# Kernel optimization log

Measured on AMD Instinct MI355X. Metric: run time of the kernel, lower is better.

Reference implementation:

```python
import jax, jax.numpy as jnp
import numpy as np

DIM = 1024
HID = 2048
OUT = 1024
NE = 8
TOPK = 2

def _xavier(key, shape):
    fan_in, fan_out = shape[-2], shape[-1]
    lim = jnp.sqrt(6.0 / (fan_in + fan_out))
    return jax.random.uniform(key, shape, jnp.float32, -lim, lim)

def setup_inputs() -> dict:
    key = jax.random.key(0)
    ks = jax.random.split(key, 8)
    X = jax.random.normal(ks[0], (4, 1024, DIM), jnp.float32)
    # stacked expert params: [NE, ...]
    W1 = _xavier(ks[1], (NE, DIM, HID))
    W3 = _xavier(ks[2], (NE, DIM, HID))
    W2 = _xavier(ks[3], (NE, HID, OUT))
    b1 = jnp.zeros((NE, HID), jnp.float32)
    b3 = jnp.zeros((NE, HID), jnp.float32)
    b2 = jnp.zeros((NE, OUT), jnp.float32)
    Wg = _xavier(ks[4], (DIM, NE))
    bg = jnp.zeros((NE,), jnp.float32)
    Wf = _xavier(ks[5], (OUT, OUT))
    bf = jnp.zeros((OUT,), jnp.float32)
    return {"X": X, "W1": W1, "b1": b1, "W3": W3, "b3": b3, "W2": W2, "b2": b2,
            "Wg": Wg, "bg": bg, "Wf": Wf, "bf": bf}

def reference(X, W1, b1, W3, b3, W2, b2, Wg, bg, Wf, bf):
    # gating: [B,S,E]
    gating = jax.nn.softmax(X @ Wg + bg, axis=-1)
    # top-k via argsort (matches original: ascending sort, take last k)
    top_k_indices = jnp.argsort(gating, axis=-1)[..., -TOPK:]  # [B,S,K]
    # dense all-expert SwiGLU FFN: [B,S,E,O]
    h1 = jnp.einsum('bsd,edh->bseh', X, W1) + b1  # [B,S,E,H]
    h3 = jnp.einsum('bsd,edh->bseh', X, W3) + b3
    h = jax.nn.silu(h1 * h3)
    expert_outputs = jnp.einsum('bseh,eho->bseo', h, W2) + b2  # [B,S,E,O]
    # gather top-k expert outputs
    topk_out = jnp.take_along_axis(expert_outputs, top_k_indices[..., None], axis=2)  # [B,S,K,O]
    topk_w = jnp.take_along_axis(gating, top_k_indices, axis=-1)  # [B,S,K]
    mixed = jnp.sum(topk_w[..., None] * topk_out, axis=2)  # [B,S,O]
    return mixed @ Wf + bf
```

## Files before the change

### kernel.cpp

```cpp
#include <hip/hip_runtime.h>

#define DIM  1024
#define HID  2048
#define OUTD 1024
#define NE   8
#define NTOK 4096

using bf16x8 = __attribute__((ext_vector_type(8))) short;
using f32x4  = __attribute__((ext_vector_type(4))) float;

__device__ __forceinline__ unsigned short f2bf(float f) {
  unsigned int u = __builtin_bit_cast(unsigned int, f);
  u += 0x7fff + ((u >> 16) & 1);
  return (unsigned short)(u >> 16);
}

__device__ __forceinline__ void gload16(const void* g, void* l) {
  __builtin_amdgcn_global_load_lds(
      (const __attribute__((address_space(1))) void*)g,
      (__attribute__((address_space(3))) void*)l, 16, 0, 0);
}

__global__ void tcast_kernel(const float* __restrict__ in,
                             unsigned short* __restrict__ out, int R, int C) {
  __shared__ float tile[32][33];
  size_t zo = (size_t)blockIdx.z * R * C;
  int c0 = blockIdx.x * 32, r0 = blockIdx.y * 32;
  int tx = threadIdx.x & 31, ty = threadIdx.x >> 5;
#pragma unroll
  for (int j = 0; j < 4; j++) {
    int r = ty + j * 8;
    tile[r][tx] = in[zo + (size_t)(r0 + r) * C + c0 + tx];
  }
  __syncthreads();
  int c = threadIdx.x >> 3, q = threadIdx.x & 7;
  ushort4 u;
  u.x = f2bf(tile[q * 4 + 0][c]); u.y = f2bf(tile[q * 4 + 1][c]);
  u.z = f2bf(tile[q * 4 + 2][c]); u.w = f2bf(tile[q * 4 + 3][c]);
  *(ushort4*)&out[zo + (size_t)(c0 + c) * R + r0 + q * 4] = u;
}

__global__ void tcast_i_kernel(const float* __restrict__ W1,
                               const float* __restrict__ W3,
                               unsigned short* __restrict__ out) {
  __shared__ float tile[32][33];
  int z = blockIdx.z, e = z & 7, s = z >> 3;
  const float* inp = (s ? W3 : W1) + (size_t)e * DIM * HID;
  unsigned short* op = out + (size_t)e * 2 * HID * DIM;
  int c0 = blockIdx.x * 32, r0 = blockIdx.y * 32;
  int tx = threadIdx.x & 31, ty = threadIdx.x >> 5;
#pragma unroll
  for (int j = 0; j < 4; j++) {
    int r = ty + j * 8;
    tile[r][tx] = inp[(size_t)(r0 + r) * HID + c0 + tx];
  }
  __syncthreads();
  int c = threadIdx.x >> 3, q = threadIdx.x & 7;
  int h = c0 + c;
  int orow = 32 * (h >> 4) + 16 * s + (h & 15);
  ushort4 u;
  u.x = f2bf(tile[q * 4 + 0][c]); u.y = f2bf(tile[q * 4 + 1][c]);
  u.z = f2bf(tile[q * 4 + 2][c]); u.w = f2bf(tile[q * 4 + 3][c]);
  *(ushort4*)&op[(size_t)orow * DIM + r0 + q * 4] = u;
}

__global__ __launch_bounds__(256) void gating_kernel(
    const float* __restrict__ X, const float* __restrict__ Wg,
    const float* __restrict__ bg, unsigned short* __restrict__ Xb,
    int* __restrict__ topk_pack, float* __restrict__ topk_w,
    int* __restrict__ blkcnt) {
  __shared__ float wgs[NE][DIM];
  __shared__ int hist[NE];
  const int tid = threadIdx.x;
  for (int d = tid; d < DIM; d += 256) {
#pragma unroll
    for (int e = 0; e < NE; e++) wgs[e][d] = Wg[d * NE + e];
  }
  if (tid < NE) hist[tid] = 0;
  __syncthreads();
  const int wave = tid >> 6, lane = tid & 63;
  for (int tk = wave; tk < 32; tk += 4) {
    const int t = blockIdx.x * 32 + tk;
    const float* xr = X + (size_t)t * DIM;
    {
      const float4* xp = (const float4*)(xr + lane * 16);
      float4 v0 = xp[0], v1 = xp[1], v2 = xp[2], v3 = xp[3];
      uint4 w0, w1;
      w0.x = f2bf(v0.x) | ((unsigned)f2bf(v0.y) << 16);
      w0.y = f2bf(v0.z) | ((unsigned)f2bf(v0.w) << 16);
      w0.z = f2bf(v1.x) | ((unsigned)f2bf(v1.y) << 16);
      w0.w = f2bf(v1.z) | ((unsigned)f2bf(v1.w) << 16);
      w1.x = f2bf(v2.x) | ((unsigned)f2bf(v2.y) << 16);
      w1.y = f2bf(v2.z) | ((unsigned)f2bf(v2.w) << 16);
      w1.z = f2bf(v3.x) | ((unsigned)f2bf(v3.y) << 16);
      w1.w = f2bf(v3.z) | ((unsigned)f2bf(v3.w) << 16);
      uint4* op = (uint4*)(Xb + (size_t)t * DIM + lane * 16);
      op[0] = w0; op[1] = w1;
    }
    float acc[NE];
#pragma unroll
    for (int e = 0; e < NE; e++) acc[e] = 0.f;
#pragma unroll
    for (int j = 0; j < 16; j++) {
      float xv = xr[lane + j * 64];
#pragma unroll
      for (int e = 0; e < NE; e++) acc[e] += xv * wgs[e][lane + j * 64];
    }
#pragma unroll
    for (int e = 0; e < NE; e++) {
#pragma unroll
      for (int off = 32; off > 0; off >>= 1) acc[e] += __shfl_xor(acc[e], off, 64);
    }
    if (lane == 0) {
      float p[NE];
      float mx = -1e30f;
#pragma unroll
      for (int e = 0; e < NE; e++) { p[e] = acc[e] + bg[e]; mx = fmaxf(mx, p[e]); }
      float s = 0.f;
#pragma unroll
      for (int e = 0; e < NE; e++) { p[e] = expf(p[e] - mx); s += p[e]; }
      float inv = 1.f / s;
#pragma unroll
      for (int e = 0; e < NE; e++) p[e] *= inv;
      int i1 = 0; float v1 = p[0];
#pragma unroll
      for (int e = 1; e < NE; e++) if (p[e] >= v1) { v1 = p[e]; i1 = e; }
      int i2 = (i1 == 0) ? 1 : 0; float v2 = p[i2];
#pragma unroll
      for (int e = 0; e < NE; e++) {
        if (e == i1) continue;
        if (p[e] >= v2 && e != i2) { v2 = p[e]; i2 = e; }
      }
      topk_pack[t] = i1 | (i2 << 4);
      topk_w[t * 2 + 0] = v1; topk_w[t * 2 + 1] = v2;
      atomicAdd(&hist[i1], 1); atomicAdd(&hist[i2], 1);
    }
  }
  __syncthreads();
  if (tid < NE) blkcnt[blockIdx.x * NE + tid] = hist[tid];
}

__global__ void prefix_kernel(const int* __restrict__ blkcnt, int* __restrict__ counts,
                              int* __restrict__ row_start, int* __restrict__ tp,
                              int* __restrict__ base) {
  const int lane = threadIdx.x;
  int tot[NE];
#pragma unroll
  for (int e = 0; e < NE; e++) {
    int s = blkcnt[lane * NE + e] + blkcnt[(lane + 64) * NE + e];
#pragma unroll
    for (int off = 32; off > 0; off >>= 1) s += __shfl_xor(s, off, 64);
    tot[e] = s;
  }
  int rsv[NE]; int s = 0, t = 0;
#pragma unroll
  for (int e = 0; e < NE; e++) {
    rsv[e] = s;
    if (lane == e) { counts[e] = tot[e]; row_start[e] = s; }
    if (lane == e) tp[e] = t;
    s += tot[e]; t += (tot[e] + 127) >> 7;
  }
  if (lane == 0) tp[NE] = t;
#pragma unroll
  for (int e = 0; e < NE; e++) {
    int c0 = blkcnt[(2 * lane) * NE + e], c1 = blkcnt[(2 * lane + 1) * NE + e];
    int s2 = c0 + c1, scan = s2;
#pragma unroll
    for (int off = 1; off < 64; off <<= 1) {
      int v = __shfl_up(scan, off, 64);
      if (lane >= off) scan += v;
    }
    int excl = scan - s2 + rsv[e];
    base[(2 * lane) * NE + e] = excl;
    base[(2 * lane + 1) * NE + e] = excl + c0;
  }
}

__global__ void scatter_kernel(const int* __restrict__ topk_pack, const int* __restrict__ base,
                               int* __restrict__ list) {
  __shared__ int lofs[NE];
  const int blk = blockIdx.x, tid = threadIdx.x;
  if (tid < NE) lofs[tid] = base[blk * NE + tid];
  __syncthreads();
  if (tid < 32) {
    int t = blk * 32 + tid;
    int pk = topk_pack[t];
    int e1 = pk & 15, e2 = (pk >> 4) & 15;
    int p1 = atomicAdd(&lofs[e1], 1);
    list[p1] = t << 1;
    int p2 = atomicAdd(&lofs[e2], 1);
    list[p2] = (t << 1) | 1;
  }
}

__global__ __launch_bounds__(256, 3) void ffn_a_kernel(
    const unsigned short* __restrict__ Xb,
    const unsigned short* __restrict__ W13t,
    const float* __restrict__ b1, const float* __restrict__ b3,
    const int* __restrict__ counts, const int* __restrict__ row_start,
    const int* __restrict__ tp, const int* __restrict__ list,
    unsigned short* __restrict__ h_buf) {
  __shared__ unsigned short As[128 * 64];
  __shared__ unsigned short Bs[128 * 64];
  const int bid = blockIdx.x;
  const int xcd = bid & 7, r = bid >> 3;
  const int grp = r >> 5, rr2 = r & 31;
  const int by = grp * 8 + (rr2 & 7);
  const int bx = xcd * 4 + (rr2 >> 3);
  if (by >= tp[NE]) return;
  int e = 0;
#pragma unroll
  for (int k = 1; k < NE; k++) if (by >= tp[k]) e = k;
  const int ne = counts[e], rs = row_start[e];
  const int m0 = (by - tp[e]) * 128;
  const int n0 = bx * 128;

  const int tid = threadIdx.x;
  const int wave = tid >> 6, lane = tid & 63;
  const int lr = lane & 15, lk = lane >> 4;
  const int wm = (wave >> 1) * 64, wn = (wave & 1) * 64;

  const int scs = ((lane & 7) ^ (lane >> 3)) * 8;
  const unsigned short* asrc[4];
  const unsigned short* bsrc[4];
#pragma unroll
  for (int i = 0; i < 4; i++) {
    int sr = (wave * 4 + i) * 8 + (lane >> 3);
    int rr = m0 + sr; if (rr >= ne) rr = m0;
    int tok = list[rs + rr] >> 1;
    asrc[i] = Xb + (size_t)tok * DIM + scs;
    bsrc[i] = W13t + ((size_t)e * 2 * HID + n0 + sr) * DIM + scs;
  }

  f32x4 acc[4][4];
  const f32x4 zero = {0.f, 0.f, 0.f, 0.f};
#pragma unroll
  for (int m = 0; m < 4; m++)
#pragma unroll
    for (int n = 0; n < 4; n++) acc[m][n] = zero;

  const int sx = lr & 7;

  for (int k0 = 0; k0 < DIM; k0 += 64) {
#pragma unroll
    for (int i = 0; i < 4; i++) {
      gload16(asrc[i] + k0, &As[(wave * 4 + i) * 512]);
      gload16(bsrc[i] + k0, &Bs[(wave * 4 + i) * 512]);
    }
    __syncthreads();
#pragma unroll
    for (int kk = 0; kk < 2; kk++) {
      const int sl = ((kk * 4 + lk) ^ sx) * 8;
      bf16x8 a[4], b[4];
#pragma unroll
      for (int m = 0; m < 4; m++)
        a[m] = *(const bf16x8*)&As[(wm + m * 16 + lr) * 64 + sl];
#pragma unroll
      for (int n = 0; n < 4; n++)
        b[n] = *(const bf16x8*)&Bs[(wn + n * 16 + lr) * 64 + sl];
#pragma unroll
      for (int m = 0; m < 4; m++)
#pragma unroll
        for (int n = 0; n < 4; n++)
          acc[m][n] = __builtin_amdgcn_mfma_f32_16x16x32_bf16(a[m], b[n], acc[m][n], 0, 0, 0);
    }
    __syncthreads();
  }

  const int hq = (n0 + wn) >> 5;
#pragma unroll
  for (int g = 0; g < 2; g++) {
    int h = (hq + g) * 16 + lr;
    float b1v = b1[e * HID + h];
    float b3v = b3[e * HID + h];
#pragma unroll
    for (int m = 0; m < 4; m++) {
#pragma unroll
      for (int j = 0; j < 4; j++) {
        int rr = m0 + wm + m * 16 + lk * 4 + j;
        if (rr < ne) {
          float h1 = acc[m][2 * g][j] + b1v;
          float h3 = acc[m][2 * g + 1][j] + b3v;
          float v = h1 * h3;
          h_buf[(size_t)(rs + rr) * HID + h] = f2bf(v / (1.f + expf(-v)));
        }
      }
    }
  }
}

__global__ __launch_bounds__(256, 3) void ffn_b_kernel(
    const unsigned short* __restrict__ h_buf,
    const unsigned short* __restrict__ W2t,
    const float* __restrict__ b2,
    const int* __restrict__ counts, const int* __restrict__ row_start,
    const int* __restrict__ tp, const int* __restrict__ list,
    const float* __restrict__ topk_w, float* __restrict__ o_buf) {
  __shared__ unsigned short As[128 * 64];
  __shared__ unsigned short Bs[128 * 64];
  const int bid = blockIdx.x;
  const int xcd = bid & 7, r = bid >> 3;
  const int grp = r / 24, rr2 = r % 24;
  const int by = xcd * 9 + grp * 3 + (rr2 % 3);
  const int bx = rr2 / 3;
  if (by >= tp[NE]) return;
  int e = 0;
#pragma unroll
  for (int k = 1; k < NE; k++) if (by >= tp[k]) e = k;
  const int ne = counts[e], rs = row_start[e];
  const int m0 = (by - tp[e]) * 128;
  const int n0 = bx * 128;

  const int tid = threadIdx.x;
  const int wave = tid >> 6, lane = tid & 63;
  const int lr = lane & 15, lk = lane >> 4;
  const int wm = (wave >> 1) * 64, wn = (wave & 1) * 64;

  const int scs = ((lane & 7) ^ (lane >> 3)) * 8;
  const unsigned short* asrc[4];
  const unsigned short* bsrc[4];
#pragma unroll
  for (int i = 0; i < 4; i++) {
    int sr = (wave * 4 + i) * 8 + (lane >> 3);
    asrc[i] = h_buf + (size_t)(rs + m0 + sr) * HID + scs;
    bsrc[i] = W2t + ((size_t)e * OUTD + n0 + sr) * HID + scs;
  }

  f32x4 acc[4][4];
  const f32x4 zero = {0.f, 0.f, 0.f, 0.f};
#pragma unroll
  for (int m = 0; m < 4; m++)
#pragma unroll
    for (int n = 0; n < 4; n++) acc[m][n] = zero;

  const int sx = lr & 7;

  for (int k0 = 0; k0 < HID; k0 += 64) {
#pragma unroll
    for (int i = 0; i < 4; i++) {
      gload16(asrc[i] + k0, &As[(wave * 4 + i) * 512]);
      gload16(bsrc[i] + k0, &Bs[(wave * 4 + i) * 512]);
    }
    __syncthreads();
#pragma unroll
    for (int kk = 0; kk < 2; kk++) {
      const int sl = ((kk * 4 + lk) ^ sx) * 8;
      bf16x8 a[4], b[4];
#pragma unroll
      for (int m = 0; m < 4; m++)
        a[m] = *(const bf16x8*)&As[(wm + m * 16 + lr) * 64 + sl];
#pragma unroll
      for (int n = 0; n < 4; n++)
        b[n] = *(const bf16x8*)&Bs[(wn + n * 16 + lr) * 64 + sl];
#pragma unroll
      for (int m = 0; m < 4; m++)
#pragma unroll
        for (int n = 0; n < 4; n++)
          acc[m][n] = __builtin_amdgcn_mfma_f32_16x16x32_bf16(a[m], b[n], acc[m][n], 0, 0, 0);
    }
    __syncthreads();
  }

#pragma unroll
  for (int n = 0; n < 4; n++) {
    int col = n0 + wn + n * 16 + lr;
    float b2v = b2[e * OUTD + col];
#pragma unroll
    for (int m = 0; m < 4; m++) {
#pragma unroll
      for (int j = 0; j < 4; j++) {
        int rr = m0 + wm + m * 16 + lk * 4 + j;
        if (rr < ne) {
          int entry = list[rs + rr];
          float w = topk_w[entry];
          o_buf[(size_t)entry * OUTD + col] = w * (acc[m][n][j] + b2v);
        }
      }
    }
  }
}

__global__ __launch_bounds__(256) void final_kernel(
    const float* __restrict__ o_buf, const unsigned short* __restrict__ Wft,
    const float* __restrict__ bfv, float* __restrict__ out) {
  const int m0 = blockIdx.y * 128, n0 = blockIdx.x * 128;

  __shared__ unsigned short As[128 * 64];
  __shared__ unsigned short Bs[128 * 64];

  const int tid = threadIdx.x;
  const int wave = tid >> 6, lane = tid & 63;
  const int lrow = lane >> 3;
  const int lcol = (lane & 7) * 8;

  const unsigned short* bsrc[4];
#pragma unroll
  for (int i = 0; i < 4; i++) {
    int sr = (wave * 4 + i) * 8 + lrow;
    bsrc[i] = Wft + (size_t)(n0 + sr) * DIM + lcol;
  }

  const int wm = (wave >> 1) * 64, wn = (wave & 1) * 64;
  const int lr = lane & 15, lk = lane >> 4;

  f32x4 acc[4][4];
  const f32x4 zero = {0.f, 0.f, 0.f, 0.f};
#pragma unroll
  for (int m = 0; m < 4; m++)
#pragma unroll
    for (int n = 0; n < 4; n++) acc[m][n] = zero;

  for (int k0 = 0; k0 < DIM; k0 += 64) {
#pragma unroll
    for (int g = 0; g < 8; g++) {
      int idx = g * 256 + tid;
      int r = idx >> 4;
      int c4 = (idx & 15) * 4;
      const float4 v0 = *(const float4*)&o_buf[(size_t)(m0 + r) * 2 * OUTD + k0 + c4];
      const float4 v1 = *(const float4*)&o_buf[(size_t)(m0 + r) * 2 * OUTD + OUTD + k0 + c4];
      ushort4 u;
      u.x = f2bf(v0.x + v1.x); u.y = f2bf(v0.y + v1.y);
      u.z = f2bf(v0.z + v1.z); u.w = f2bf(v0.w + v1.w);
      *(ushort4*)&As[r * 64 + c4] = u;
    }
#pragma unroll
    for (int i = 0; i < 4; i++) gload16(bsrc[i] + k0, &Bs[(wave * 4 + i) * 512]);
    __syncthreads();
#pragma unroll
    for (int kk = 0; kk < 2; kk++) {
      bf16x8 a[4], b[4];
#pragma unroll
      for (int m = 0; m < 4; m++)
        a[m] = *(const bf16x8*)&As[(wm + m * 16 + lr) * 64 + kk * 32 + lk * 8];
#pragma unroll
      for (int n = 0; n < 4; n++)
        b[n] = *(const bf16x8*)&Bs[(wn + n * 16 + lr) * 64 + kk * 32 + lk * 8];
#pragma unroll
      for (int m = 0; m < 4; m++)
#pragma unroll
        for (int n = 0; n < 4; n++)
          acc[m][n] = __builtin_amdgcn_mfma_f32_16x16x32_bf16(a[m], b[n], acc[m][n], 0, 0, 0);
    }
    __syncthreads();
  }

#pragma unroll
  for (int n = 0; n < 4; n++) {
    int col = n0 + wn + n * 16 + lr;
    float bv = bfv[col];
#pragma unroll
    for (int m = 0; m < 4; m++) {
#pragma unroll
      for (int j = 0; j < 4; j++) {
        int r = m0 + wm + m * 16 + lk * 4 + j;
        out[(size_t)r * OUTD + col] = acc[m][n][j] + bv;
      }
    }
  }
}

extern "C" void kernel_launch(void* const* d_in, const int* in_sizes, int n_in,
                              void* d_out, int out_size, void* d_ws, size_t ws_size,
                              hipStream_t stream) {
  const float* X   = (const float*)d_in[0];
  const float* W1  = (const float*)d_in[1];
  const float* b1  = (const float*)d_in[2];
  const float* W3  = (const float*)d_in[3];
  const float* b3  = (const float*)d_in[4];
  const float* W2  = (const float*)d_in[5];
  const float* b2  = (const float*)d_in[6];
  const float* Wg  = (const float*)d_in[7];
  const float* bg  = (const float*)d_in[8];
  const float* Wf  = (const float*)d_in[9];
  const float* bfv = (const float*)d_in[10];
  float* out = (float*)d_out;

  char* p = (char*)d_ws;
  auto alloc = [&](size_t bytes) { char* r = p; p += (bytes + 255) & ~(size_t)255; return r; };
  unsigned short* Xb   = (unsigned short*)alloc((size_t)NTOK * DIM * 2);
  unsigned short* W13t = (unsigned short*)alloc((size_t)NE * 2 * HID * DIM * 2);
  unsigned short* W2t  = (unsigned short*)alloc((size_t)NE * OUTD * HID * 2);
  unsigned short* Wft  = (unsigned short*)alloc((size_t)OUTD * DIM * 2);
  unsigned short* hbuf = (unsigned short*)alloc((size_t)(NTOK * 2 + 256) * HID * 2);
  float* o_buf         = (float*)alloc((size_t)NTOK * 2 * OUTD * 4);
  int* topk_pack       = (int*)alloc(NTOK * 4);
  float* topk_w        = (float*)alloc(NTOK * 2 * 4);
  int* counts          = (int*)alloc(NE * 4);
  int* row_start       = (int*)alloc(NE * 4);
  int* tp              = (int*)alloc((NE + 1) * 4);
  int* blkcnt          = (int*)alloc(128 * NE * 4);
  int* base            = (int*)alloc(128 * NE * 4);
  int* list            = (int*)alloc(NTOK * 2 * 4);

  gating_kernel<<<128, 256, 0, stream>>>(X, Wg, bg, Xb, topk_pack, topk_w, blkcnt);
  tcast_i_kernel<<<dim3(HID / 32, DIM / 32, 16), 256, 0, stream>>>(W1, W3, W13t);
  tcast_kernel<<<dim3(OUTD / 32, HID / 32, NE), 256, 0, stream>>>(W2, W2t, HID, OUTD);
  tcast_kernel<<<dim3(OUTD / 32, DIM / 32, 1), 256, 0, stream>>>(Wf, Wft, DIM, OUTD);

  prefix_kernel<<<1, 64, 0, stream>>>(blkcnt, counts, row_start, tp, base);
  scatter_kernel<<<128, 64, 0, stream>>>(topk_pack, base, list);

  ffn_a_kernel<<<2304, 256, 0, stream>>>(
      Xb, W13t, b1, b3, counts, row_start, tp, list, hbuf);
  ffn_b_kernel<<<576, 256, 0, stream>>>(
      hbuf, W2t, b2, counts, row_start, tp, list, topk_w, o_buf);
  final_kernel<<<dim3(OUTD / 128, NTOK / 128), 256, 0, stream>>>(o_buf, Wft, bfv, out);
}
```

Measured before the change: 302.7 us.

## Fuse prep kernels, merge prefix into scatter, triple-buffer GEMM k-loops

Gating and the W1/W3 transpose-cast now run in one launch, and the W2/Wf transpose-casts ride as extra blocks inside the ffn_a launch. The prefix kernel is folded into scatter, which computes per-block offsets redundantly. Both expert GEMMs now use a 32-wide k-step with a 3-stage LDS ring driven by explicit vmcnt waits, replacing the 64-wide single-buffered loop. The XCD-aware block swizzle is dropped, and sizing the LDS ring also to hold the fp32 transpose tile may lower occupancy.

```diff
diff --git a/kernel.cpp b/kernel.cpp
--- a/kernel.cpp
+++ b/kernel.cpp
@@ -21,56 +21,49 @@
       (__attribute__((address_space(3))) void*)l, 16, 0, 0);
 }
 
-__global__ void tcast_kernel(const float* __restrict__ in,
-                             unsigned short* __restrict__ out, int R, int C) {
-  __shared__ float tile[32][33];
-  size_t zo = (size_t)blockIdx.z * R * C;
-  int c0 = blockIdx.x * 32, r0 = blockIdx.y * 32;
+#define BARR __builtin_amdgcn_s_barrier()
+#define VMC8 asm volatile("s_waitcnt vmcnt(8)" ::: "memory")
+#define VMC4 asm volatile("s_waitcnt vmcnt(4)" ::: "memory")
+#define VMC0 asm volatile("s_waitcnt vmcnt(0)" ::: "memory")
+
+__device__ __forceinline__ void tcast_body(const float* __restrict__ inp,
+                                           unsigned short* __restrict__ op,
+                                           int R, int C, int c0, int r0,
+                                           float (*tile)[33], int interleave, int s) {
   int tx = threadIdx.x & 31, ty = threadIdx.x >> 5;
 #pragma unroll
-  for (int j = 0; j < 4; j++) {
-    int r = ty + j * 8;
-    tile[r][tx] = in[zo + (size_t)(r0 + r) * C + c0 + tx];
-  }
+  for (int j = 0; j < 4; j++)
+    tile[ty + j * 8][tx] = inp[(size_t)(r0 + ty + j * 8) * C + c0 + tx];
   __syncthreads();
   int c = threadIdx.x >> 3, q = threadIdx.x & 7;
+  int h = c0 + c;
+  int orow = interleave ? (32 * (h >> 4) + 16 * s + (h & 15)) : h;
   ushort4 u;
   u.x = f2bf(tile[q * 4 + 0][c]); u.y = f2bf(tile[q * 4 + 1][c]);
   u.z = f2bf(tile[q * 4 + 2][c]); u.w = f2bf(tile[q * 4 + 3][c]);
-  *(ushort4*)&out[zo + (size_t)(c0 + c) * R + r0 + q * 4] = u;
-}
-
-__global__ void tcast_i_kernel(const float* __restrict__ W1,
-                               const float* __restrict__ W3,
-                               unsigned short* __restrict__ out) {
-  __shared__ float tile[32][33];
-  int z = blockIdx.z, e = z & 7, s = z >> 3;
-  const float* inp = (s ? W3 : W1) + (size_t)e * DIM * HID;
-  unsigned short* op = out + (size_t)e * 2 * HID * DIM;
-  int c0 = blockIdx.x * 32, r0 = blockIdx.y * 32;
-  int tx = threadIdx.x & 31, ty = threadIdx.x >> 5;
-#pragma unroll
-  for (int j = 0; j < 4; j++) {
-    int r = ty + j * 8;
-    tile[r][tx] = inp[(size_t)(r0 + r) * HID + c0 + tx];
-  }
-  __syncthreads();
-  int c = threadIdx.x >> 3, q = threadIdx.x & 7;
-  int h = c0 + c;
-  int orow = 32 * (h >> 4) + 16 * s + (h & 15);
-  ushort4 u;
-  u.x = f2bf(tile[q * 4 + 0][c]); u.y = f2bf(tile[q * 4 + 1][c]);
-  u.z = f2bf(tile[q * 4 + 2][c]); u.w = f2bf(tile[q * 4 + 3][c]);
-  *(ushort4*)&op[(size_t)orow * DIM + r0 + q * 4] = u;
-}
-
-__global__ __launch_bounds__(256) void gating_kernel(
+  *(ushort4*)&op[(size_t)orow * R + r0 + q * 4] = u;
+}
+
+__global__ __launch_bounds__(256) void prep_kernel(
     const float* __restrict__ X, const float* __restrict__ Wg,
-    const float* __restrict__ bg, unsigned short* __restrict__ Xb,
-    int* __restrict__ topk_pack, float* __restrict__ topk_w,
-    int* __restrict__ blkcnt) {
-  __shared__ float wgs[NE][DIM];
-  __shared__ int hist[NE];
+    const float* __restrict__ bg, const float* __restrict__ W1,
+    const float* __restrict__ W3, unsigned short* __restrict__ Xb,
+    unsigned short* __restrict__ W13t, int* __restrict__ topk_pack,
+    float* __restrict__ topk_w, int* __restrict__ blkcnt) {
+  __shared__ float smem[NE * DIM + NE];
+  const int b = blockIdx.x;
+  if (b >= 128) {
+    int z = (b - 128) >> 11;
+    int rem = (b - 128) & 2047;
+    int bx = rem & 63, byy = rem >> 6;
+    int e = z & 7, s = z >> 3;
+    const float* inp = (s ? W3 : W1) + (size_t)e * DIM * HID;
+    unsigned short* op = W13t + (size_t)e * 2 * HID * DIM;
+    tcast_body(inp, op, DIM, HID, bx * 32, byy * 32, (float(*)[33])smem, 1, s);
+    return;
+  }
+  float (*wgs)[DIM] = (float(*)[DIM])smem;
+  int* hist = (int*)&smem[NE * DIM];
   const int tid = threadIdx.x;
   for (int d = tid; d < DIM; d += 256) {
 #pragma unroll
@@ -80,7 +73,7 @@
   __syncthreads();
   const int wave = tid >> 6, lane = tid & 63;
   for (int tk = wave; tk < 32; tk += 4) {
-    const int t = blockIdx.x * 32 + tk;
+    const int t = b * 32 + tk;
     const float* xr = X + (size_t)t * DIM;
     {
       const float4* xp = (const float4*)(xr + lane * 16);
@@ -94,8 +87,8 @@
       w1.y = f2bf(v2.z) | ((unsigned)f2bf(v2.w) << 16);
       w1.z = f2bf(v3.x) | ((unsigned)f2bf(v3.y) << 16);
       w1.w = f2bf(v3.z) | ((unsigned)f2bf(v3.w) << 16);
-      uint4* op = (uint4*)(Xb + (size_t)t * DIM + lane * 16);
-      op[0] = w0; op[1] = w1;
+      uint4* op2 = (uint4*)(Xb + (size_t)t * DIM + lane * 16);
+      op2[0] = w0; op2[1] = w1;
     }
     float acc[NE];
 #pragma unroll
@@ -116,10 +109,10 @@
       float mx = -1e30f;
 #pragma unroll
       for (int e = 0; e < NE; e++) { p[e] = acc[e] + bg[e]; mx = fmaxf(mx, p[e]); }
-      float s = 0.f;
-#pragma unroll
-      for (int e = 0; e < NE; e++) { p[e] = expf(p[e] - mx); s += p[e]; }
-      float inv = 1.f / s;
+      float sum = 0.f;
+#pragma unroll
+      for (int e = 0; e < NE; e++) { p[e] = expf(p[e] - mx); sum += p[e]; }
+      float inv = 1.f / sum;
 #pragma unroll
       for (int e = 0; e < NE; e++) p[e] *= inv;
       int i1 = 0; float v1 = p[0];
@@ -137,76 +130,69 @@
     }
   }
   __syncthreads();
-  if (tid < NE) blkcnt[blockIdx.x * NE + tid] = hist[tid];
-}
-
-__global__ void prefix_kernel(const int* __restrict__ blkcnt, int* __restrict__ counts,
-                              int* __restrict__ row_start, int* __restrict__ tp,
-                              int* __restrict__ base) {
+  if (tid < NE) blkcnt[b * NE + tid] = hist[tid];
+}
+
+__global__ void scatter_kernel(const int* __restrict__ blkcnt,
+                               const int* __restrict__ topk_pack,
+                               int* __restrict__ counts, int* __restrict__ row_start,
+                               int* __restrict__ tp, int* __restrict__ list) {
+  __shared__ int lofs[NE];
   const int lane = threadIdx.x;
-  int tot[NE];
+  const int myb = blockIdx.x;
+  int s = 0, t = 0;
 #pragma unroll
   for (int e = 0; e < NE; e++) {
-    int s = blkcnt[lane * NE + e] + blkcnt[(lane + 64) * NE + e];
-#pragma unroll
-    for (int off = 32; off > 0; off >>= 1) s += __shfl_xor(s, off, 64);
-    tot[e] = s;
-  }
-  int rsv[NE]; int s = 0, t = 0;
-#pragma unroll
-  for (int e = 0; e < NE; e++) {
-    rsv[e] = s;
-    if (lane == e) { counts[e] = tot[e]; row_start[e] = s; }
-    if (lane == e) tp[e] = t;
-    s += tot[e]; t += (tot[e] + 127) >> 7;
-  }
-  if (lane == 0) tp[NE] = t;
-#pragma unroll
-  for (int e = 0; e < NE; e++) {
-    int c0 = blkcnt[(2 * lane) * NE + e], c1 = blkcnt[(2 * lane + 1) * NE + e];
-    int s2 = c0 + c1, scan = s2;
-#pragma unroll
-    for (int off = 1; off < 64; off <<= 1) {
-      int v = __shfl_up(scan, off, 64);
-      if (lane >= off) scan += v;
-    }
-    int excl = scan - s2 + rsv[e];
-    base[(2 * lane) * NE + e] = excl;
-    base[(2 * lane + 1) * NE + e] = excl + c0;
-  }
-}
-
-__global__ void scatter_kernel(const int* __restrict__ topk_pack, const int* __restrict__ base,
-                               int* __restrict__ list) {
-  __shared__ int lofs[NE];
-  const int blk = blockIdx.x, tid = threadIdx.x;
-  if (tid < NE) lofs[tid] = base[blk * NE + tid];
+    int c0 = blkcnt[lane * NE + e], c1 = blkcnt[(lane + 64) * NE + e];
+    int tote = c0 + c1;
+    int pre = (lane < myb ? c0 : 0) + (lane + 64 < myb ? c1 : 0);
+#pragma unroll
+    for (int off = 32; off > 0; off >>= 1) {
+      tote += __shfl_xor(tote, off, 64);
+      pre  += __shfl_xor(pre,  off, 64);
+    }
+    if (lane == 0) lofs[e] = s + pre;
+    if (myb == 0 && lane == 0) { counts[e] = tote; row_start[e] = s; tp[e] = t; }
+    s += tote; t += (tote + 127) >> 7;
+  }
+  if (myb == 0 && lane == 0) tp[NE] = t;
   __syncthreads();
-  if (tid < 32) {
-    int t = blk * 32 + tid;
-    int pk = topk_pack[t];
+  if (lane < 32) {
+    int tok = myb * 32 + lane;
+    int pk = topk_pack[tok];
     int e1 = pk & 15, e2 = (pk >> 4) & 15;
-    int p1 = atomicAdd(&lofs[e1], 1);
-    list[p1] = t << 1;
-    int p2 = atomicAdd(&lofs[e2], 1);
-    list[p2] = (t << 1) | 1;
-  }
-}
-
+    int p1 = atomicAdd(&lofs[e1], 1); list[p1] = tok << 1;
+    int p2 = atomicAdd(&lofs[e2], 1); list[p2] = (tok << 1) | 1;
+  }
+}
+
+#define FFNA_BLKS 2304
+#define W2T_BLKS  16384
 __global__ __launch_bounds__(256, 3) void ffn_a_kernel(
     const unsigned short* __restrict__ Xb,
     const unsigned short* __restrict__ W13t,
     const float* __restrict__ b1, const float* __restrict__ b3,
+    const float* __restrict__ W2, const float* __restrict__ Wf,
+    unsigned short* __restrict__ W2t, unsigned short* __restrict__ Wft,
     const int* __restrict__ counts, const int* __restrict__ row_start,
     const int* __restrict__ tp, const int* __restrict__ list,
     unsigned short* __restrict__ h_buf) {
-  __shared__ unsigned short As[128 * 64];
-  __shared__ unsigned short Bs[128 * 64];
-  const int bid = blockIdx.x;
-  const int xcd = bid & 7, r = bid >> 3;
-  const int grp = r >> 5, rr2 = r & 31;
-  const int by = grp * 8 + (rr2 & 7);
-  const int bx = xcd * 4 + (rr2 >> 3);
+  __shared__ unsigned short As[3 * 8192];
+  const int b = blockIdx.x;
+  if (b >= FFNA_BLKS) {
+    if (b < FFNA_BLKS + W2T_BLKS) {
+      int z = (b - FFNA_BLKS) >> 11, rem = (b - FFNA_BLKS) & 2047;
+      int bx = rem & 31, byy = rem >> 5;
+      tcast_body(W2 + (size_t)z * HID * OUTD, W2t + (size_t)z * OUTD * HID,
+                 HID, OUTD, bx * 32, byy * 32, (float(*)[33])As, 0, 0);
+    } else {
+      int z = b - FFNA_BLKS - W2T_BLKS;
+      int bx = z & 31, byy = z >> 5;
+      tcast_body(Wf, Wft, DIM, OUTD, bx * 32, byy * 32, (float(*)[33])As, 0, 0);
+    }
+    return;
+  }
+  const int bx = b & 31, by = b >> 5;
   if (by >= tp[NE]) return;
   int e = 0;
 #pragma unroll
@@ -220,12 +206,14 @@
   const int lr = lane & 15, lk = lane >> 4;
   const int wm = (wave >> 1) * 64, wn = (wave & 1) * 64;
 
-  const int scs = ((lane & 7) ^ (lane >> 3)) * 8;
-  const unsigned short* asrc[4];
-  const unsigned short* bsrc[4];
-#pragma unroll
-  for (int i = 0; i < 4; i++) {
-    int sr = (wave * 4 + i) * 8 + (lane >> 3);
+  const int srow = wave * 16 + (lane >> 2);
+  const int sxs = (srow >> 1) & 3;
+  const int scs = ((lane & 3) ^ sxs) * 8;
+  const unsigned short* asrc[2];
+  const unsigned short* bsrc[2];
+#pragma unroll
+  for (int i = 0; i < 2; i++) {
+    int sr = i * 64 + srow;
     int rr = m0 + sr; if (rr >= ne) rr = m0;
     int tok = list[rs + rr] >> 1;
     asrc[i] = Xb + (size_t)tok * DIM + scs;
@@ -239,33 +227,48 @@
 #pragma unroll
     for (int n = 0; n < 4; n++) acc[m][n] = zero;
 
-  const int sx = lr & 7;
-
-  for (int k0 = 0; k0 < DIM; k0 += 64) {
-#pragma unroll
-    for (int i = 0; i < 4; i++) {
-      gload16(asrc[i] + k0, &As[(wave * 4 + i) * 512]);
-      gload16(bsrc[i] + k0, &Bs[(wave * 4 + i) * 512]);
-    }
-    __syncthreads();
-#pragma unroll
-    for (int kk = 0; kk < 2; kk++) {
-      const int sl = ((kk * 4 + lk) ^ sx) * 8;
-      bf16x8 a[4], b[4];
-#pragma unroll
-      for (int m = 0; m < 4; m++)
-        a[m] = *(const bf16x8*)&As[(wm + m * 16 + lr) * 64 + sl];
+  auto STAGE = [&](int t, int buf) {
+    unsigned short* p = As + buf * 8192 + wave * 512;
+    const int ko = t * 32;
+    gload16(asrc[0] + ko, p);
+    gload16(asrc[1] + ko, p + 2048);
+    gload16(bsrc[0] + ko, p + 4096);
+    gload16(bsrc[1] + ko, p + 6144);
+  };
+  const int sxr = (lr >> 1) & 3;
+  auto COMPUTE = [&](int buf) {
+    const unsigned short* Ab = As + buf * 8192;
+    const unsigned short* Bb = Ab + 4096;
+    bf16x8 a[4], bv[4];
+#pragma unroll
+    for (int m = 0; m < 4; m++) {
+      int row = wm + m * 16 + lr;
+      a[m] = *(const bf16x8*)&Ab[row * 32 + ((lk ^ sxr) * 8)];
+    }
+#pragma unroll
+    for (int n = 0; n < 4; n++) {
+      int row = wn + n * 16 + lr;
+      bv[n] = *(const bf16x8*)&Bb[row * 32 + ((lk ^ sxr) * 8)];
+    }
+#pragma unroll
+    for (int m = 0; m < 4; m++)
 #pragma unroll
       for (int n = 0; n < 4; n++)
-        b[n] = *(const bf16x8*)&Bs[(wn + n * 16 + lr) * 64 + sl];
-#pragma unroll
-      for (int m = 0; m < 4; m++)
-#pragma unroll
-        for (int n = 0; n < 4; n++)
-          acc[m][n] = __builtin_amdgcn_mfma_f32_16x16x32_bf16(a[m], b[n], acc[m][n], 0, 0, 0);
-    }
-    __syncthreads();
-  }
+        acc[m][n] = __builtin_amdgcn_mfma_f32_16x16x32_bf16(a[m], bv[n], acc[m][n], 0, 0, 0);
+  };
+
+  const int NT = DIM / 32;
+  STAGE(0, 0); STAGE(1, 1);
+#define AITER(t, CUR, NX)                                   \
+  if ((t) + 2 < NT) { STAGE((t) + 2, NX); VMC8; }           \
+  else if ((t) + 1 < NT) { VMC4; } else { VMC0; }           \
+  BARR; COMPUTE(CUR); BARR;
+  for (int t = 0; t < NT; t += 3) {
+    AITER(t, 0, 2);
+    if (t + 1 < NT) { AITER(t + 1, 1, 0); }
+    if (t + 2 < NT) { AITER(t + 2, 2, 1); }
+  }
+#undef AITER
 
   const int hq = (n0 + wn) >> 5;
 #pragma unroll
@@ -296,32 +299,29 @@
     const int* __restrict__ counts, const int* __restrict__ row_start,
     const int* __restrict__ tp, const int* __restrict__ list,
     const float* __restrict__ topk_w, float* __restrict__ o_buf) {
-  __shared__ unsigned short As[128 * 64];
-  __shared__ unsigned short Bs[128 * 64];
-  const int bid = blockIdx.x;
-  const int xcd = bid & 7, r = bid >> 3;
-  const int grp = r / 24, rr2 = r % 24;
-  const int by = xcd * 9 + grp * 3 + (rr2 % 3);
-  const int bx = rr2 / 3;
+  __shared__ unsigned short As[3 * 8192];
+  const int by = blockIdx.y;
   if (by >= tp[NE]) return;
   int e = 0;
 #pragma unroll
   for (int k = 1; k < NE; k++) if (by >= tp[k]) e = k;
   const int ne = counts[e], rs = row_start[e];
   const int m0 = (by - tp[e]) * 128;
-  const int n0 = bx * 128;
+  const int n0 = blockIdx.x * 128;
 
   const int tid = threadIdx.x;
   const int wave = tid >> 6, lane = tid & 63;
   const int lr = lane & 15, lk = lane >> 4;
   const int wm = (wave >> 1) * 64, wn = (wave & 1) * 64;
 
-  const int scs = ((lane & 7) ^ (lane >> 3)) * 8;
-  const unsigned short* asrc[4];
-  const unsigned short* bsrc[4];
-#pragma unroll
-  for (int i = 0; i < 4; i++) {
-    int sr = (wave * 4 + i) * 8 + (lane >> 3);
+  const int srow = wave * 16 + (lane >> 2);
+  const int sxs = (srow >> 1) & 3;
+  const int scs = ((lane & 3) ^ sxs) * 8;
+  const unsigned short* asrc[2];
+  const unsigned short* bsrc[2];
+#pragma unroll
+  for (int i = 0; i < 2; i++) {
+    int sr = i * 64 + srow;
     asrc[i] = h_buf + (size_t)(rs + m0 + sr) * HID + scs;
     bsrc[i] = W2t + ((size_t)e * OUTD + n0 + sr) * HID + scs;
   }
@@ -333,33 +333,48 @@
 #pragma unroll
     for (int n = 0; n < 4; n++) acc[m][n] = zero;
 
-  const int sx = lr & 7;
-
-  for (int k0 = 0; k0 < HID; k0 += 64) {
-#pragma unroll
-    for (int i = 0; i < 4; i++) {
-      gload16(asrc[i] + k0, &As[(wave * 4 + i) * 512]);
-      gload16(bsrc[i] + k0, &Bs[(wave * 4 + i) * 512]);
-    }
-    __syncthreads();
-#pragma unroll
-    for (int kk = 0; kk < 2; kk++) {
-      const int sl = ((kk * 4 + lk) ^ sx) * 8;
-      bf16x8 a[4], b[4];
-#pragma unroll
-      for (int m = 0; m < 4; m++)
-        a[m] = *(const bf16x8*)&As[(wm + m * 16 + lr) * 64 + sl];
+  auto STAGE = [&](int t, int buf) {
+    unsigned short* p = As + buf * 8192 + wave * 512;
+    const int ko = t * 32;
+    gload16(asrc[0] + ko, p);
+    gload16(asrc[1] + ko, p + 2048);
+    gload16(bsrc[0] + ko, p + 4096);
+    gload16(bsrc[1] + ko, p + 6144);
+  };
+  const int sxr = (lr >> 1) & 3;
+  auto COMPUTE = [&](int buf) {
+    const unsigned short* Ab = As + buf * 8192;
+    const unsigned short* Bb = Ab + 4096;
+    bf16x8 a[4], bv[4];
+#pragma unroll
+    for (int m = 0; m < 4; m++) {
+      int row = wm + m * 16 + lr;
+      a[m] = *(const bf16x8*)&Ab[row * 32 + ((lk ^ sxr) * 8)];
+    }
+#pragma unroll
+    for (int n = 0; n < 4; n++) {
+      int row = wn + n * 16 + lr;
+      bv[n] = *(const bf16x8*)&Bb[row * 32 + ((lk ^ sxr) * 8)];
+    }
+#pragma unroll
+    for (int m = 0; m < 4; m++)
 #pragma unroll
       for (int n = 0; n < 4; n++)
-        b[n] = *(const bf16x8*)&Bs[(wn + n * 16 + lr) * 64 + sl];
-#pragma unroll
-      for (int m = 0; m < 4; m++)
-#pragma unroll
-        for (int n = 0; n < 4; n++)
-          acc[m][n] = __builtin_amdgcn_mfma_f32_16x16x32_bf16(a[m], b[n], acc[m][n], 0, 0, 0);
-    }
-    __syncthreads();
-  }
+        acc[m][n] = __builtin_amdgcn_mfma_f32_16x16x32_bf16(a[m], bv[n], acc[m][n], 0, 0, 0);
+  };
+
+  const int NT = HID / 32;
+  STAGE(0, 0); STAGE(1, 1);
+#define BITER(t, CUR, NX)                                   \
+  if ((t) + 2 < NT) { STAGE((t) + 2, NX); VMC8; }           \
+  else if ((t) + 1 < NT) { VMC4; } else { VMC0; }           \
+  BARR; COMPUTE(CUR); BARR;
+  for (int t = 0; t < NT; t += 3) {
+    BITER(t, 0, 2);
+    if (t + 1 < NT) { BITER(t + 1, 1, 0); }
+    if (t + 2 < NT) { BITER(t + 2, 2, 1); }
+  }
+#undef BITER
 
 #pragma unroll
   for (int n = 0; n < 4; n++) {
@@ -489,20 +504,14 @@
   int* row_start       = (int*)alloc(NE * 4);
   int* tp              = (int*)alloc((NE + 1) * 4);
   int* blkcnt          = (int*)alloc(128 * NE * 4);
-  int* base            = (int*)alloc(128 * NE * 4);
   int* list            = (int*)alloc(NTOK * 2 * 4);
 
-  gating_kernel<<<128, 256, 0, stream>>>(X, Wg, bg, Xb, topk_pack, topk_w, blkcnt);
-  tcast_i_kernel<<<dim3(HID / 32, DIM / 32, 16), 256, 0, stream>>>(W1, W3, W13t);
-  tcast_kernel<<<dim3(OUTD / 32, HID / 32, NE), 256, 0, stream>>>(W2, W2t, HID, OUTD);
-  tcast_kernel<<<dim3(OUTD / 32, DIM / 32, 1), 256, 0, stream>>>(Wf, Wft, DIM, OUTD);
-
-  prefix_kernel<<<1, 64, 0, stream>>>(blkcnt, counts, row_start, tp, base);
-  scatter_kernel<<<128, 64, 0, stream>>>(topk_pack, base, list);
-
-  ffn_a_kernel<<<2304, 256, 0, stream>>>(
-      Xb, W13t, b1, b3, counts, row_start, tp, list, hbuf);
-  ffn_b_kernel<<<576, 256, 0, stream>>>(
+  prep_kernel<<<128 + 32768, 256, 0, stream>>>(
+      X, Wg, bg, W1, W3, Xb, W13t, topk_pack, topk_w, blkcnt);
+  scatter_kernel<<<128, 64, 0, stream>>>(blkcnt, topk_pack, counts, row_start, tp, list);
+  ffn_a_kernel<<<FFNA_BLKS + W2T_BLKS + 1024, 256, 0, stream>>>(
+      Xb, W13t, b1, b3, W2, Wf, W2t, Wft, counts, row_start, tp, list, hbuf);
+  ffn_b_kernel<<<dim3(OUTD / 128, 72), 256, 0, stream>>>(
       hbuf, W2t, b2, counts, row_start, tp, list, topk_w, o_buf);
   final_kernel<<<dim3(OUTD / 128, NTOK / 128), 256, 0, stream>>>(o_buf, Wft, bfv, out);
 }
```

New measurement: 306.2 us. About the same (+1.2%).

## Merge small kernels, enlarge FFN-A tile, store expert outputs in bf16

Applied to the files above, without the earlier changes.

Merges the two weight-transpose kernels into one launch and folds the prefix scan into the scatter kernel, which removes launch overheads. FFN-A moves to 512-thread blocks with a 128x256 tile so each A tile is reused across more columns. Per-expert outputs are now stored as bf16 rather than fp32, halving the intermediate traffic into the final GEMM. The XCD-aware block swizzles in FFN-A and FFN-B are replaced by plain 2D grids, and the final kernel gets a new block ordering. The bf16 intermediate adds rounding error, and the larger tile lowers the number of resident blocks.

```diff
diff --git a/kernel.cpp b/kernel.cpp
--- a/kernel.cpp
+++ b/kernel.cpp
@@ -14,6 +14,10 @@
   u += 0x7fff + ((u >> 16) & 1);
   return (unsigned short)(u >> 16);
 }
+__device__ __forceinline__ float b2f(unsigned short u) {
+  unsigned int v = (unsigned int)u << 16;
+  return __builtin_bit_cast(float, v);
+}
 
 __device__ __forceinline__ void gload16(const void* g, void* l) {
   __builtin_amdgcn_global_load_lds(
@@ -21,23 +25,22 @@
       (__attribute__((address_space(3))) void*)l, 16, 0, 0);
 }
 
-__global__ void tcast_kernel(const float* __restrict__ in,
-                             unsigned short* __restrict__ out, int R, int C) {
-  __shared__ float tile[32][33];
-  size_t zo = (size_t)blockIdx.z * R * C;
-  int c0 = blockIdx.x * 32, r0 = blockIdx.y * 32;
+__device__ __forceinline__ void tc_tile(const float* __restrict__ inp, int C,
+                                        unsigned short* __restrict__ op, int R,
+                                        int c0, int r0, float (*tile)[33],
+                                        int interleave, int s) {
   int tx = threadIdx.x & 31, ty = threadIdx.x >> 5;
 #pragma unroll
-  for (int j = 0; j < 4; j++) {
-    int r = ty + j * 8;
-    tile[r][tx] = in[zo + (size_t)(r0 + r) * C + c0 + tx];
-  }
+  for (int j = 0; j < 4; j++)
+    tile[ty + j * 8][tx] = inp[(size_t)(r0 + ty + j * 8) * C + c0 + tx];
   __syncthreads();
   int c = threadIdx.x >> 3, q = threadIdx.x & 7;
+  int h = c0 + c;
+  int orow = interleave ? (32 * (h >> 4) + 16 * s + (h & 15)) : h;
   ushort4 u;
   u.x = f2bf(tile[q * 4 + 0][c]); u.y = f2bf(tile[q * 4 + 1][c]);
   u.z = f2bf(tile[q * 4 + 2][c]); u.w = f2bf(tile[q * 4 + 3][c]);
-  *(ushort4*)&out[zo + (size_t)(c0 + c) * R + r0 + q * 4] = u;
+  *(ushort4*)&op[(size_t)orow * R + r0 + q * 4] = u;
 }
 
 __global__ void tcast_i_kernel(const float* __restrict__ W1,
@@ -47,21 +50,21 @@
   int z = blockIdx.z, e = z & 7, s = z >> 3;
   const float* inp = (s ? W3 : W1) + (size_t)e * DIM * HID;
   unsigned short* op = out + (size_t)e * 2 * HID * DIM;
-  int c0 = blockIdx.x * 32, r0 = blockIdx.y * 32;
-  int tx = threadIdx.x & 31, ty = threadIdx.x >> 5;
-#pragma unroll
-  for (int j = 0; j < 4; j++) {
-    int r = ty + j * 8;
-    tile[r][tx] = inp[(size_t)(r0 + r) * HID + c0 + tx];
-  }
-  __syncthreads();
-  int c = threadIdx.x >> 3, q = threadIdx.x & 7;
-  int h = c0 + c;
-  int orow = 32 * (h >> 4) + 16 * s + (h & 15);
-  ushort4 u;
-  u.x = f2bf(tile[q * 4 + 0][c]); u.y = f2bf(tile[q * 4 + 1][c]);
-  u.z = f2bf(tile[q * 4 + 2][c]); u.w = f2bf(tile[q * 4 + 3][c]);
-  *(ushort4*)&op[(size_t)orow * DIM + r0 + q * 4] = u;
+  tc_tile(inp, HID, op, DIM, blockIdx.x * 32, blockIdx.y * 32, tile, 1, s);
+}
+
+__global__ void tcast2_kernel(const float* __restrict__ W2, const float* __restrict__ Wf,
+                              unsigned short* __restrict__ W2t,
+                              unsigned short* __restrict__ Wft) {
+  __shared__ float tile[32][33];
+  int z = blockIdx.z;
+  if (z < NE) {
+    tc_tile(W2 + (size_t)z * HID * OUTD, OUTD, W2t + (size_t)z * OUTD * HID, HID,
+            blockIdx.x * 32, blockIdx.y * 32, tile, 0, 0);
+  } else {
+    if (blockIdx.y >= DIM / 32) return;
+    tc_tile(Wf, OUTD, Wft, DIM, blockIdx.x * 32, blockIdx.y * 32, tile, 0, 0);
+  }
 }
 
 __global__ __launch_bounds__(256) void gating_kernel(
@@ -94,8 +97,8 @@
       w1.y = f2bf(v2.z) | ((unsigned)f2bf(v2.w) << 16);
       w1.z = f2bf(v3.x) | ((unsigned)f2bf(v3.y) << 16);
       w1.w = f2bf(v3.z) | ((unsigned)f2bf(v3.w) << 16);
-      uint4* op = (uint4*)(Xb + (size_t)t * DIM + lane * 16);
-      op[0] = w0; op[1] = w1;
+      uint4* op2 = (uint4*)(Xb + (size_t)t * DIM + lane * 16);
+      op2[0] = w0; op2[1] = w1;
     }
     float acc[NE];
 #pragma unroll
@@ -116,10 +119,10 @@
       float mx = -1e30f;
 #pragma unroll
       for (int e = 0; e < NE; e++) { p[e] = acc[e] + bg[e]; mx = fmaxf(mx, p[e]); }
-      float s = 0.f;
-#pragma unroll
-      for (int e = 0; e < NE; e++) { p[e] = expf(p[e] - mx); s += p[e]; }
-      float inv = 1.f / s;
+      float sum = 0.f;
+#pragma unroll
+      for (int e = 0; e < NE; e++) { p[e] = expf(p[e] - mx); sum += p[e]; }
+      float inv = 1.f / sum;
 #pragma unroll
       for (int e = 0; e < NE; e++) p[e] *= inv;
       int i1 = 0; float v1 = p[0];
@@ -140,96 +143,75 @@
   if (tid < NE) blkcnt[blockIdx.x * NE + tid] = hist[tid];
 }
 
-__global__ void prefix_kernel(const int* __restrict__ blkcnt, int* __restrict__ counts,
-                              int* __restrict__ row_start, int* __restrict__ tp,
-                              int* __restrict__ base) {
+__global__ void scatter_kernel(const int* __restrict__ blkcnt,
+                               const int* __restrict__ topk_pack,
+                               int* __restrict__ counts, int* __restrict__ row_start,
+                               int* __restrict__ tp, int* __restrict__ list) {
+  __shared__ int lofs[NE];
   const int lane = threadIdx.x;
-  int tot[NE];
+  const int myb = blockIdx.x;
+  int s = 0, t = 0;
 #pragma unroll
   for (int e = 0; e < NE; e++) {
-    int s = blkcnt[lane * NE + e] + blkcnt[(lane + 64) * NE + e];
-#pragma unroll
-    for (int off = 32; off > 0; off >>= 1) s += __shfl_xor(s, off, 64);
-    tot[e] = s;
-  }
-  int rsv[NE]; int s = 0, t = 0;
-#pragma unroll
-  for (int e = 0; e < NE; e++) {
-    rsv[e] = s;
-    if (lane == e) { counts[e] = tot[e]; row_start[e] = s; }
-    if (lane == e) tp[e] = t;
-    s += tot[e]; t += (tot[e] + 127) >> 7;
-  }
-  if (lane == 0) tp[NE] = t;
-#pragma unroll
-  for (int e = 0; e < NE; e++) {
-    int c0 = blkcnt[(2 * lane) * NE + e], c1 = blkcnt[(2 * lane + 1) * NE + e];
-    int s2 = c0 + c1, scan = s2;
-#pragma unroll
-    for (int off = 1; off < 64; off <<= 1) {
-      int v = __shfl_up(scan, off, 64);
-      if (lane >= off) scan += v;
-    }
-    int excl = scan - s2 + rsv[e];
-    base[(2 * lane) * NE + e] = excl;
-    base[(2 * lane + 1) * NE + e] = excl + c0;
-  }
-}
-
-__global__ void scatter_kernel(const int* __restrict__ topk_pack, const int* __restrict__ base,
-                               int* __restrict__ list) {
-  __shared__ int lofs[NE];
-  const int blk = blockIdx.x, tid = threadIdx.x;
-  if (tid < NE) lofs[tid] = base[blk * NE + tid];
+    int c0 = blkcnt[lane * NE + e], c1 = blkcnt[(lane + 64) * NE + e];
+    int tote = c0 + c1;
+    int pre = (lane < myb ? c0 : 0) + (lane + 64 < myb ? c1 : 0);
+#pragma unroll
+    for (int off = 32; off > 0; off >>= 1) {
+      tote += __shfl_xor(tote, off, 64);
+      pre  += __shfl_xor(pre,  off, 64);
+    }
+    if (lane == 0) lofs[e] = s + pre;
+    if (myb == 0 && lane == 0) { counts[e] = tote; row_start[e] = s; tp[e] = t; }
+    s += tote; t += (tote + 127) >> 7;
+  }
+  if (myb == 0 && lane == 0) tp[NE] = t;
   __syncthreads();
-  if (tid < 32) {
-    int t = blk * 32 + tid;
-    int pk = topk_pack[t];
+  if (lane < 32) {
+    int tok = myb * 32 + lane;
+    int pk = topk_pack[tok];
     int e1 = pk & 15, e2 = (pk >> 4) & 15;
-    int p1 = atomicAdd(&lofs[e1], 1);
-    list[p1] = t << 1;
-    int p2 = atomicAdd(&lofs[e2], 1);
-    list[p2] = (t << 1) | 1;
-  }
-}
-
-__global__ __launch_bounds__(256, 3) void ffn_a_kernel(
+    int p1 = atomicAdd(&lofs[e1], 1); list[p1] = tok << 1;
+    int p2 = atomicAdd(&lofs[e2], 1); list[p2] = (tok << 1) | 1;
+  }
+}
+
+__global__ __launch_bounds__(512, 4) void ffn_a_kernel(
     const unsigned short* __restrict__ Xb,
     const unsigned short* __restrict__ W13t,
     const float* __restrict__ b1, const float* __restrict__ b3,
     const int* __restrict__ counts, const int* __restrict__ row_start,
     const int* __restrict__ tp, const int* __restrict__ list,
     unsigned short* __restrict__ h_buf) {
-  __shared__ unsigned short As[128 * 64];
-  __shared__ unsigned short Bs[128 * 64];
-  const int bid = blockIdx.x;
-  const int xcd = bid & 7, r = bid >> 3;
-  const int grp = r >> 5, rr2 = r & 31;
-  const int by = grp * 8 + (rr2 & 7);
-  const int bx = xcd * 4 + (rr2 >> 3);
+  __shared__ unsigned short S[24576];
+  const int by = blockIdx.y;
   if (by >= tp[NE]) return;
   int e = 0;
 #pragma unroll
   for (int k = 1; k < NE; k++) if (by >= tp[k]) e = k;
   const int ne = counts[e], rs = row_start[e];
   const int m0 = (by - tp[e]) * 128;
-  const int n0 = bx * 128;
+  const int n0 = blockIdx.x * 256;
 
   const int tid = threadIdx.x;
   const int wave = tid >> 6, lane = tid & 63;
   const int lr = lane & 15, lk = lane >> 4;
-  const int wm = (wave >> 1) * 64, wn = (wave & 1) * 64;
+  const int wm = (wave & 1) * 64, wn = (wave >> 1) * 64;
 
   const int scs = ((lane & 7) ^ (lane >> 3)) * 8;
-  const unsigned short* asrc[4];
+  const unsigned short* asrc[2];
   const unsigned short* bsrc[4];
 #pragma unroll
-  for (int i = 0; i < 4; i++) {
-    int sr = (wave * 4 + i) * 8 + (lane >> 3);
+  for (int i = 0; i < 2; i++) {
+    int sr = i * 64 + wave * 8 + (lane >> 3);
     int rr = m0 + sr; if (rr >= ne) rr = m0;
     int tok = list[rs + rr] >> 1;
     asrc[i] = Xb + (size_t)tok * DIM + scs;
-    bsrc[i] = W13t + ((size_t)e * 2 * HID + n0 + sr) * DIM + scs;
+  }
+#pragma unroll
+  for (int c = 0; c < 4; c++) {
+    int sr = c * 64 + wave * 8 + (lane >> 3);
+    bsrc[c] = W13t + ((size_t)e * 2 * HID + n0 + sr) * DIM + scs;
   }
 
   f32x4 acc[4][4];
@@ -243,10 +225,11 @@
 
   for (int k0 = 0; k0 < DIM; k0 += 64) {
 #pragma unroll
-    for (int i = 0; i < 4; i++) {
-      gload16(asrc[i] + k0, &As[(wave * 4 + i) * 512]);
-      gload16(bsrc[i] + k0, &Bs[(wave * 4 + i) * 512]);
-    }
+    for (int i = 0; i < 2; i++)
+      gload16(asrc[i] + k0, &S[(i * 64 + wave * 8) * 64]);
+#pragma unroll
+    for (int c = 0; c < 4; c++)
+      gload16(bsrc[c] + k0, &S[8192 + (c * 64 + wave * 8) * 64]);
     __syncthreads();
 #pragma unroll
     for (int kk = 0; kk < 2; kk++) {
@@ -254,10 +237,10 @@
       bf16x8 a[4], b[4];
 #pragma unroll
       for (int m = 0; m < 4; m++)
-        a[m] = *(const bf16x8*)&As[(wm + m * 16 + lr) * 64 + sl];
+        a[m] = *(const bf16x8*)&S[(wm + m * 16 + lr) * 64 + sl];
 #pragma unroll
       for (int n = 0; n < 4; n++)
-        b[n] = *(const bf16x8*)&Bs[(wn + n * 16 + lr) * 64 + sl];
+        b[n] = *(const bf16x8*)&S[8192 + (wn + n * 16 + lr) * 64 + sl];
 #pragma unroll
       for (int m = 0; m < 4; m++)
 #pragma unroll
@@ -295,21 +278,17 @@
     const float* __restrict__ b2,
     const int* __restrict__ counts, const int* __restrict__ row_start,
     const int* __restrict__ tp, const int* __restrict__ list,
-    const float* __restrict__ topk_w, float* __restrict__ o_buf) {
+    const float* __restrict__ topk_w, unsigned short* __restrict__ ob) {
   __shared__ unsigned short As[128 * 64];
   __shared__ unsigned short Bs[128 * 64];
-  const int bid = blockIdx.x;
-  const int xcd = bid & 7, r = bid >> 3;
-  const int grp = r / 24, rr2 = r % 24;
-  const int by = xcd * 9 + grp * 3 + (rr2 % 3);
-  const int bx = rr2 / 3;
+  const int by = blockIdx.y;
   if (by >= tp[NE]) return;
   int e = 0;
 #pragma unroll
   for (int k = 1; k < NE; k++) if (by >= tp[k]) e = k;
   const int ne = counts[e], rs = row_start[e];
   const int m0 = (by - tp[e]) * 128;
-  const int n0 = bx * 128;
+  const int n0 = blockIdx.x * 128;
 
   const int tid = threadIdx.x;
   const int wave = tid >> 6, lane = tid & 63;
@@ -373,7 +352,7 @@
         if (rr < ne) {
           int entry = list[rs + rr];
           float w = topk_w[entry];
-          o_buf[(size_t)entry * OUTD + col] = w * (acc[m][n][j] + b2v);
+          ob[(size_t)entry * OUTD + col] = f2bf(w * (acc[m][n][j] + b2v));
         }
       }
     }
@@ -381,9 +360,11 @@
 }
 
 __global__ __launch_bounds__(256) void final_kernel(
-    const float* __restrict__ o_buf, const unsigned short* __restrict__ Wft,
+    const unsigned short* __restrict__ ob, const unsigned short* __restrict__ Wft,
     const float* __restrict__ bfv, float* __restrict__ out) {
-  const int m0 = blockIdx.y * 128, n0 = blockIdx.x * 128;
+  const int bid = blockIdx.x;
+  const int n0 = (bid >> 5) * 128;
+  const int m0 = ((bid & 7) + 8 * ((bid >> 3) & 3)) * 128;
 
   __shared__ unsigned short As[128 * 64];
   __shared__ unsigned short Bs[128 * 64];
@@ -416,11 +397,11 @@
       int idx = g * 256 + tid;
       int r = idx >> 4;
       int c4 = (idx & 15) * 4;
-      const float4 v0 = *(const float4*)&o_buf[(size_t)(m0 + r) * 2 * OUTD + k0 + c4];
-      const float4 v1 = *(const float4*)&o_buf[(size_t)(m0 + r) * 2 * OUTD + OUTD + k0 + c4];
+      ushort4 a0 = *(const ushort4*)&ob[((size_t)(m0 + r) * 2) * OUTD + k0 + c4];
+      ushort4 a1 = *(const ushort4*)&ob[((size_t)(m0 + r) * 2 + 1) * OUTD + k0 + c4];
       ushort4 u;
-      u.x = f2bf(v0.x + v1.x); u.y = f2bf(v0.y + v1.y);
-      u.z = f2bf(v0.z + v1.z); u.w = f2bf(v0.w + v1.w);
+      u.x = f2bf(b2f(a0.x) + b2f(a1.x)); u.y = f2bf(b2f(a0.y) + b2f(a1.y));
+      u.z = f2bf(b2f(a0.z) + b2f(a1.z)); u.w = f2bf(b2f(a0.w) + b2f(a1.w));
       *(ushort4*)&As[r * 64 + c4] = u;
     }
 #pragma unroll
@@ -482,27 +463,24 @@
   unsigned short* W2t  = (unsigned short*)alloc((size_t)NE * OUTD * HID * 2);
   unsigned short* Wft  = (unsigned short*)alloc((size_t)OUTD * DIM * 2);
   unsigned short* hbuf = (unsigned short*)alloc((size_t)(NTOK * 2 + 256) * HID * 2);
-  float* o_buf         = (float*)alloc((size_t)NTOK * 2 * OUTD * 4);
+  unsigned short* ob   = (unsigned short*)alloc((size_t)NTOK * 2 * OUTD * 2);
   int* topk_pack       = (int*)alloc(NTOK * 4);
   float* topk_w        = (float*)alloc(NTOK * 2 * 4);
   int* counts          = (int*)alloc(NE * 4);
   int* row_start       = (int*)alloc(NE * 4);
   int* tp              = (int*)alloc((NE + 1) * 4);
   int* blkcnt          = (int*)alloc(128 * NE * 4);
-  int* base            = (int*)alloc(128 * NE * 4);
   int* list            = (int*)alloc(NTOK * 2 * 4);
 
   gating_kernel<<<128, 256, 0, stream>>>(X, Wg, bg, Xb, topk_pack, topk_w, blkcnt);
   tcast_i_kernel<<<dim3(HID / 32, DIM / 32, 16), 256, 0, stream>>>(W1, W3, W13t);
-  tcast_kernel<<<dim3(OUTD / 32, HID / 32, NE), 256, 0, stream>>>(W2, W2t, HID, OUTD);
-  tcast_kernel<<<dim3(OUTD / 32, DIM / 32, 1), 256, 0, stream>>>(Wf, Wft, DIM, OUTD);
-
-  prefix_kernel<<<1, 64, 0, stream>>>(blkcnt, counts, row_start, tp, base);
-  scatter_kernel<<<128, 64, 0, stream>>>(topk_pack, base, list);
-
-  ffn_a_kernel<<<2304, 256, 0, stream>>>(
+  tcast2_kernel<<<dim3(OUTD / 32, HID / 32, NE + 1), 256, 0, stream>>>(W2, Wf, W2t, Wft);
+
+  scatter_kernel<<<128, 64, 0, stream>>>(blkcnt, topk_pack, counts, row_start, tp, list);
+
+  ffn_a_kernel<<<dim3(2 * HID / 256, 72), 512, 0, stream>>>(
       Xb, W13t, b1, b3, counts, row_start, tp, list, hbuf);
-  ffn_b_kernel<<<576, 256, 0, stream>>>(
-      hbuf, W2t, b2, counts, row_start, tp, list, topk_w, o_buf);
-  final_kernel<<<dim3(OUTD / 128, NTOK / 128), 256, 0, stream>>>(o_buf, Wft, bfv, out);
-}
+  ffn_b_kernel<<<dim3(OUTD / 128, 72), 256, 0, stream>>>(
+      hbuf, W2t, b2, counts, row_start, tp, list, topk_w, ob);
+  final_kernel<<<256, 256, 0, stream>>>(ob, Wft, bfv, out);
+}
```

Result: slower. 315.8 us (+4.3%).
